# Performance work log

Hardware: AMD Instinct MI355X
Metric: run time of the kernel (lower is better)

## Reference

```python
import jax, jax.numpy as jnp
import numpy as np

NUM_HEADS = 12


def setup_inputs() -> dict:
    key = jax.random.key(0)
    k1, k2, k3, k4 = jax.random.split(key, 4)
    B, N, C = 8, 1024, 768
    x = jax.random.normal(k1, (B, N, C), dtype=jnp.float32)
    w_qkv = jax.random.normal(k2, (3 * C, C), dtype=jnp.float32) * 0.02
    w_proj = jax.random.normal(k3, (C, C), dtype=jnp.float32) * 0.02
    b_proj = jax.random.normal(k4, (C,), dtype=jnp.float32) * 0.02
    return {"x": x, "w_qkv": w_qkv, "w_proj": w_proj, "b_proj": b_proj}


def reference(x, w_qkv, w_proj, b_proj):
    B, N, C = x.shape
    H = NUM_HEADS
    D = C // H
    scale = D ** -0.5
    # qkv projection (HMQLinear with quant=False is a plain linear, bias=False)
    qkv = jnp.einsum('bnc,oc->bno', x, w_qkv)          # [B,N,3C]
    qkv = qkv.reshape(B, N, 3, H, D).transpose(2, 0, 3, 1, 4)  # [3,B,H,N,D]
    q, k, v = qkv[0], qkv[1], qkv[2]
    # HMQMulQK (passthrough matmul), scale applied after QK^T as in source
    attn = jnp.einsum('bhqd,bhkd->bhqk', q, k) * scale  # [B,H,N,N]
    attn = jax.nn.softmax(attn, axis=-1)                # HMQSoftmax
    out = jnp.einsum('bhqk,bhkd->bhqd', attn, v)        # HMQMulSV
    out = out.transpose(0, 2, 1, 3).reshape(B, N, C)
    # output projection (HMQLinear, default bias=True)
    return jnp.einsum('bnc,oc->bno', out, w_proj) + b_proj
```

## Files before the change

kernel.cpp:

```cpp
#include <hip/hip_runtime.h>
#include <hip/hip_bf16.h>
#include <stdint.h>

typedef __attribute__((ext_vector_type(8))) short short8;
typedef __attribute__((ext_vector_type(4))) float f32x4;
typedef __attribute__((ext_vector_type(16))) float f32x16;
typedef __attribute__((ext_vector_type(4))) unsigned short us4;

#define AS1 __attribute__((address_space(1)))
#define AS3 __attribute__((address_space(3)))

__device__ inline unsigned short f2bf(float f) {
    unsigned int u = __float_as_uint(f);
    u += 0x7FFFu + ((u >> 16) & 1u);
    return (unsigned short)(u >> 16);
}

__device__ inline unsigned int cvtpk(float lo, float hi) {
    unsigned int r;
    asm("v_cvt_pk_bf16_f32 %0, %1, %2" : "=v"(r) : "v"(lo), "v"(hi));
    return r;
}

__device__ inline void pl32swap(unsigned int& a, unsigned int& b) {
    asm volatile("v_permlane32_swap_b32 %0, %1" : "+v"(a), "+v"(b));
}

__device__ inline float fexp2(float x) {
#if __has_builtin(__builtin_amdgcn_exp2f)
    return __builtin_amdgcn_exp2f(x);
#else
    return exp2f(x);
#endif
}

#define VMW(N) asm volatile("s_waitcnt vmcnt(" #N ")" ::: "memory")
#define BARR() __builtin_amdgcn_s_barrier()

__global__ void cvt_all(const float* __restrict__ x, const float* __restrict__ wq,
                        const float* __restrict__ wp,
                        unsigned short* __restrict__ xb,
                        unsigned short* __restrict__ wqb,
                        unsigned short* __restrict__ wpb) {
    const int X4 = 1572864, Q4 = 442368;
    int i = blockIdx.x * blockDim.x + threadIdx.x;
    const float* src; unsigned short* dst; int j;
    if (i < X4) { src = x; dst = xb; j = i; }
    else if (i < X4 + Q4) { src = wq; dst = wqb; j = i - X4; }
    else { src = wp; dst = wpb; j = i - X4 - Q4; }
    float4 v = ((const float4*)src)[j];
    us4 o;
    o.x = f2bf(v.x); o.y = f2bf(v.y); o.z = f2bf(v.z); o.w = f2bf(v.w);
    ((us4*)dst)[j] = o;
}

#define BM 128
#define BN 128

template<int MODE>
__global__ __launch_bounds__(256)
void gemm_bt(const unsigned short* __restrict__ A,
             const unsigned short* __restrict__ Bm,
             unsigned short* __restrict__ Qo, unsigned short* __restrict__ Ko,
             unsigned short* __restrict__ Vto,
             float* __restrict__ Co, const float* __restrict__ bias,
             int M, int N, int K)
{
    __shared__ __align__(16) unsigned short As[2][BM * 64];
    __shared__ __align__(16) unsigned short Bs[2][BM * 64];
    const int tid = threadIdx.x;
    const int wave = tid >> 6, lane = tid & 63;
    const int tr = blockIdx.x * BM;
    const int tc = blockIdx.y * BN;
    const int wm = wave >> 1, wn = wave & 1;

    f32x4 acc[4][4] = {};

    auto stage = [&](int it, int buf) {
#pragma unroll
        for (int i = 0; i < 4; ++i) {
            int cid = i * 256 + tid;
            int r = cid >> 3, cd = cid & 7;
            int sc = cd ^ (r & 7);
            __builtin_amdgcn_global_load_lds(
                (const AS1 void*)(A + (size_t)(tr + r) * K + it * 64 + sc * 8),
                (AS3 void*)(&As[buf][(i * 256 + wave * 64) * 8]), 16, 0, 0);
            __builtin_amdgcn_global_load_lds(
                (const AS1 void*)(Bm + (size_t)(tc + r) * K + it * 64 + sc * 8),
                (AS3 void*)(&Bs[buf][(i * 256 + wave * 64) * 8]), 16, 0, 0);
        }
    };

    const int nIt = K / 64;
    stage(0, 0);

    for (int it = 0; it < nIt; ++it) {
        const int cur = it & 1;
        if (it + 1 < nIt) { stage(it + 1, cur ^ 1); VMW(8); }
        else              { VMW(0); }
        BARR();

#pragma unroll
        for (int kh = 0; kh < 2; ++kh) {
            short8 af[4], bfr[4];
#pragma unroll
            for (int mt = 0; mt < 4; ++mt) {
                int rr = wm * 64 + mt * 16 + (lane & 15);
                int c = kh * 4 + (lane >> 4);
                af[mt] = *(const short8*)&As[cur][rr * 64 + ((c ^ (rr & 7)) * 8)];
            }
#pragma unroll
            for (int nt = 0; nt < 4; ++nt) {
                int rr = wn * 64 + nt * 16 + (lane & 15);
                int c = kh * 4 + (lane >> 4);
                bfr[nt] = *(const short8*)&Bs[cur][rr * 64 + ((c ^ (rr & 7)) * 8)];
            }
#pragma unroll
            for (int mt = 0; mt < 4; ++mt)
#pragma unroll
                for (int nt = 0; nt < 4; ++nt)
                    acc[mt][nt] = __builtin_amdgcn_mfma_f32_16x16x32_bf16(af[mt], bfr[nt], acc[mt][nt], 0, 0, 0);
        }

        BARR();
    }

    const float QSCALE = 0.18033688011112042f;
#pragma unroll
    for (int mt = 0; mt < 4; ++mt) {
#pragma unroll
        for (int nt = 0; nt < 4; ++nt) {
            int col = tc + wn * 64 + nt * 16 + (lane & 15);
            int row0 = tr + wm * 64 + mt * 16 + (lane >> 4) * 4;
            if constexpr (MODE == 0) {
                int s = (col >= 1536) ? 2 : (col >= 768 ? 1 : 0);
                int rem = col - s * 768;
                int h = rem >> 6, d = rem & 63;
                int b = row0 >> 10, n0 = row0 & 1023;
                int bh = b * 12 + h;
                if (s == 2) {
                    us4 pv;
#pragma unroll
                    for (int r = 0; r < 4; ++r) pv[r] = f2bf(acc[mt][nt][r]);
                    int qd = (n0 >> 2) & 3;
                    int nst = n0 + ((qd == 1) ? 4 : (qd == 2) ? -4 : 0);
                    *(us4*)&Vto[((size_t)bh * 64 + d) * 1024 + nst] = pv;
                } else {
                    unsigned short* dst = (s == 0) ? Qo : Ko;
                    float sc = (s == 0) ? QSCALE : 1.0f;
#pragma unroll
                    for (int r = 0; r < 4; ++r)
                        dst[((size_t)bh * 1024 + n0 + r) * 64 + d] = f2bf(acc[mt][nt][r] * sc);
                }
            } else {
#pragma unroll
                for (int r = 0; r < 4; ++r)
                    Co[(size_t)(row0 + r) * N + col] = acc[mt][nt][r] + bias[col];
            }
        }
    }
}

__global__ __launch_bounds__(256, 3)
void attn_kernel(const unsigned short* __restrict__ Q,
                 const unsigned short* __restrict__ Kg,
                 const unsigned short* __restrict__ Vt,
                 unsigned short* __restrict__ Og)
{
    __shared__ __align__(16) unsigned short KV[3][2][64 * 64];

    const int tid = threadIdx.x;
    const int wave = tid >> 6, lane = tid & 63;
    const int l31 = lane & 31, hi = lane >> 5;

    const int id = blockIdx.x;
    const int swz = (id & 7) * 96 + (id >> 3);
    const int bh = swz >> 3, qb = swz & 7;

    const int b = bh / 12, h = bh % 12;
    const size_t baseK = (size_t)bh * 1024 * 64;
    const size_t baseV = (size_t)bh * 64 * 1024;
    const int q0 = qb * 128 + wave * 32;

    short8 qf[4];
#pragma unroll
    for (int ds = 0; ds < 4; ++ds)
        qf[ds] = *(const short8*)&Q[baseK + (size_t)(q0 + l31) * 64 + ds * 16 + hi * 8];

    f32x16 ot0 = {}, ot1 = {};
    float l = 0.f;

    auto stage = [&](int kt, int buf) {
        const unsigned short* gK = Kg + baseK + (size_t)kt * 64 * 64;
        const unsigned short* gV = Vt + baseV + kt * 64;
#pragma unroll
        for (int i = 0; i < 2; ++i) {
            int c = wave * 128 + i * 64 + lane;
            int r = c >> 3, cc = c & 7;
            int sw = (cc ^ (r & 7)) * 8;
            __builtin_amdgcn_global_load_lds(
                (const AS1 void*)(gK + r * 64 + sw),
                (AS3 void*)(&KV[buf][0][(wave * 128 + i * 64) * 8]), 16, 0, 0);
            __builtin_amdgcn_global_load_lds(
                (const AS1 void*)(gV + (size_t)r * 1024 + sw),
                (AS3 void*)(&KV[buf][1][(wave * 128 + i * 64) * 8]), 16, 0, 0);
        }
    };

    auto rfrag = [&](const unsigned short* s, int row, int cc) -> short8 {
        return *(const short8*)&s[(row * 8 + (cc ^ (row & 7))) * 8];
    };

    auto pack8 = [&](const f32x16& S, int r0) -> short8 {
        union { unsigned int u[4]; short8 s; } fr;
#pragma unroll
        for (int w = 0; w < 4; ++w)
            fr.u[w] = cvtpk(S[r0 + 2 * w], S[r0 + 2 * w + 1]);
        return fr.s;
    };

    stage(0, 0);
    stage(1, 1);
    int cb = 0, sb = 2;

    for (int kt = 0; kt < 16; ++kt) {
        if (kt < 15) { VMW(4); }
        else         { VMW(0); }
        BARR();
        if (kt < 14) stage(kt + 2, sb);

        f32x16 st0 = {}, st1 = {};
        __builtin_amdgcn_s_setprio(1);
#pragma unroll
        for (int ds = 0; ds < 4; ++ds) {
            short8 k0 = rfrag(KV[cb][0], l31, ds * 2 + hi);
            short8 k1 = rfrag(KV[cb][0], 32 + l31, ds * 2 + hi);
            st0 = __builtin_amdgcn_mfma_f32_32x32x16_bf16(k0, qf[ds], st0, 0, 0, 0);
            st1 = __builtin_amdgcn_mfma_f32_32x32x16_bf16(k1, qf[ds], st1, 0, 0, 0);
        }
        __builtin_amdgcn_s_setprio(0);

        short8 v00 = rfrag(KV[cb][1], l31, 0 + hi);
        short8 v10 = rfrag(KV[cb][1], 32 + l31, 0 + hi);
        short8 v01 = rfrag(KV[cb][1], l31, 2 + hi);
        short8 v11 = rfrag(KV[cb][1], 32 + l31, 2 + hi);

#pragma unroll
        for (int i = 0; i < 16; ++i) st0[i] = fexp2(st0[i]);
        short8 paf0 = pack8(st0, 0);
        short8 paf1 = pack8(st0, 8);

        __builtin_amdgcn_s_setprio(1);
        ot0 = __builtin_amdgcn_mfma_f32_32x32x16_bf16(v00, paf0, ot0, 0, 0, 0);
        ot1 = __builtin_amdgcn_mfma_f32_32x32x16_bf16(v10, paf0, ot1, 0, 0, 0);
        ot0 = __builtin_amdgcn_mfma_f32_32x32x16_bf16(v01, paf1, ot0, 0, 0, 0);
        ot1 = __builtin_amdgcn_mfma_f32_32x32x16_bf16(v11, paf1, ot1, 0, 0, 0);
        __builtin_amdgcn_s_setprio(0);

        short8 v02 = rfrag(KV[cb][1], l31, 4 + hi);
        short8 v12 = rfrag(KV[cb][1], 32 + l31, 4 + hi);
        short8 v03 = rfrag(KV[cb][1], l31, 6 + hi);
        short8 v13 = rfrag(KV[cb][1], 32 + l31, 6 + hi);
#pragma unroll
        for (int i = 0; i < 16; ++i) st1[i] = fexp2(st1[i]);
        short8 paf2 = pack8(st1, 0);
        short8 paf3 = pack8(st1, 8);

        __builtin_amdgcn_s_setprio(1);
        ot0 = __builtin_amdgcn_mfma_f32_32x32x16_bf16(v02, paf2, ot0, 0, 0, 0);
        ot1 = __builtin_amdgcn_mfma_f32_32x32x16_bf16(v12, paf2, ot1, 0, 0, 0);
        ot0 = __builtin_amdgcn_mfma_f32_32x32x16_bf16(v03, paf3, ot0, 0, 0, 0);
        ot1 = __builtin_amdgcn_mfma_f32_32x32x16_bf16(v13, paf3, ot1, 0, 0, 0);
        __builtin_amdgcn_s_setprio(0);

        float su[8];
#pragma unroll
        for (int i = 0; i < 8; ++i)
            su[i] = (st0[2 * i] + st0[2 * i + 1]) + (st1[2 * i] + st1[2 * i + 1]);
#pragma unroll
        for (int s = 4; s > 0; s >>= 1)
#pragma unroll
            for (int i = 0; i < 4; ++i)
                if (i < s) su[i] += su[i + s];
        l += su[0];

        cb = (cb == 2) ? 0 : cb + 1;
        sb = (sb == 2) ? 0 : sb + 1;
    }

    {
        unsigned int pu = __float_as_uint(l), pv = pu;
        pl32swap(pu, pv);
        l += __uint_as_float(hi ? pv : pu);
    }

    float inv = 1.f / l;
#pragma unroll
    for (int i = 0; i < 16; ++i) { ot0[i] *= inv; ot1[i] *= inv; }

    BARR();

    unsigned int* ow = (unsigned int*)(&KV[0][0][0]) + wave * 1152;
#pragma unroll
    for (int dt = 0; dt < 2; ++dt)
#pragma unroll
        for (int rp = 0; rp < 8; ++rp) {
            unsigned int w = (dt == 0) ? cvtpk(ot0[2 * rp], ot0[2 * rp + 1])
                                       : cvtpk(ot1[2 * rp], ot1[2 * rp + 1]);
            int wd = dt * 16 + 4 * (rp >> 1) + 2 * hi + (rp & 1);
            ow[l31 * 36 + wd] = w;
        }
#pragma unroll
    for (int i = 0; i < 4; ++i) {
        int c = i * 64 + lane;
        int qr = c >> 3, ch = c & 7;
        short8 vv = *(const short8*)((const unsigned short*)&ow[qr * 36 + ch * 4]);
        *(short8*)&Og[(size_t)(b * 1024 + q0 + qr) * 768 + h * 64 + ch * 8] = vv;
    }
}

extern "C" void kernel_launch(void* const* d_in, const int* in_sizes, int n_in,
                              void* d_out, int out_size, void* d_ws, size_t ws_size,
                              hipStream_t stream) {
    const float* x      = (const float*)d_in[0];
    const float* w_qkv  = (const float*)d_in[1];
    const float* w_proj = (const float*)d_in[2];
    const float* b_proj = (const float*)d_in[3];
    float* out = (float*)d_out;

    const int Bb = 8, Nn = 1024, C = 768;
    const int M = Bb * Nn;
    const size_t XB = (size_t)M * C;
    const size_t WQ = (size_t)3 * C * C;
    const size_t WP = (size_t)C * C;
    const size_t QE = (size_t)96 * 1024 * 64;

    unsigned short* xb  = (unsigned short*)d_ws;
    unsigned short* wqb = xb + XB;
    unsigned short* wpb = wqb + WQ;
    unsigned short* Qb  = wpb + WP;
    unsigned short* Kb  = Qb + QE;
    unsigned short* Vtb = Kb + QE;
    unsigned short* AO  = Vtb + QE;

    cvt_all<<<8448, 256, 0, stream>>>(x, w_qkv, w_proj, xb, wqb, wpb);

    gemm_bt<0><<<dim3(M / BM, (3 * C) / BN), 256, 0, stream>>>(
        xb, wqb, Qb, Kb, Vtb, nullptr, nullptr, M, 3 * C, C);

    attn_kernel<<<768, 256, 0, stream>>>(Qb, Kb, Vtb, AO);

    gemm_bt<1><<<dim3(M / BM, C / BN), 256, 0, stream>>>(
        AO, wpb, nullptr, nullptr, nullptr, out, b_proj, M, C, C);
}
```

Before: 109.5 us.

## Process two 32-row query tiles per wave in attention, halving block size

The attention block drops from four waves to two, and each wave now handles 64 query rows as two 32-row groups. Each K/V fragment read from LDS is reused across both groups, which halves LDS fragment traffic per unit of MFMA work and gives more independent MFMAs to interleave. The cost is a roughly doubled set of accumulator and score registers per wave (launch bounds change to 128,2), fewer waves per block to hide latency, and each wave issuing twice as many staging loads.

Measured after the change: 112.0 us. 2.3% more time.

```diff
diff --git a/kernel.cpp b/kernel.cpp
--- a/kernel.cpp
+++ b/kernel.cpp
@@ -161,7 +161,7 @@
     }
 }
 
-__global__ __launch_bounds__(256, 3)
+__global__ __launch_bounds__(128, 2)
 void attn_kernel(const unsigned short* __restrict__ Q,
                  const unsigned short* __restrict__ Kg,
                  const unsigned short* __restrict__ Vt,
@@ -180,30 +180,33 @@
     const int b = bh / 12, h = bh % 12;
     const size_t baseK = (size_t)bh * 1024 * 64;
     const size_t baseV = (size_t)bh * 64 * 1024;
-    const int q0 = qb * 128 + wave * 32;
-
-    short8 qf[4];
-#pragma unroll
-    for (int ds = 0; ds < 4; ++ds)
-        qf[ds] = *(const short8*)&Q[baseK + (size_t)(q0 + l31) * 64 + ds * 16 + hi * 8];
-
-    f32x16 ot0 = {}, ot1 = {};
-    float l = 0.f;
+    const int q0A = qb * 128 + wave * 64;
+    const int q0B = q0A + 32;
+
+    short8 qfA[4], qfB[4];
+#pragma unroll
+    for (int ds = 0; ds < 4; ++ds) {
+        qfA[ds] = *(const short8*)&Q[baseK + (size_t)(q0A + l31) * 64 + ds * 16 + hi * 8];
+        qfB[ds] = *(const short8*)&Q[baseK + (size_t)(q0B + l31) * 64 + ds * 16 + hi * 8];
+    }
+
+    f32x16 oA0 = {}, oA1 = {}, oB0 = {}, oB1 = {};
+    float lA = 0.f, lB = 0.f;
 
     auto stage = [&](int kt, int buf) {
         const unsigned short* gK = Kg + baseK + (size_t)kt * 64 * 64;
         const unsigned short* gV = Vt + baseV + kt * 64;
 #pragma unroll
-        for (int i = 0; i < 2; ++i) {
-            int c = wave * 128 + i * 64 + lane;
+        for (int i = 0; i < 4; ++i) {
+            int c = i * 128 + wave * 64 + lane;
             int r = c >> 3, cc = c & 7;
             int sw = (cc ^ (r & 7)) * 8;
             __builtin_amdgcn_global_load_lds(
                 (const AS1 void*)(gK + r * 64 + sw),
-                (AS3 void*)(&KV[buf][0][(wave * 128 + i * 64) * 8]), 16, 0, 0);
+                (AS3 void*)(&KV[buf][0][(i * 128 + wave * 64) * 8]), 16, 0, 0);
             __builtin_amdgcn_global_load_lds(
                 (const AS1 void*)(gV + (size_t)r * 1024 + sw),
-                (AS3 void*)(&KV[buf][1][(wave * 128 + i * 64) * 8]), 16, 0, 0);
+                (AS3 void*)(&KV[buf][1][(i * 128 + wave * 64) * 8]), 16, 0, 0);
         }
     };
 
@@ -224,98 +227,115 @@
     int cb = 0, sb = 2;
 
     for (int kt = 0; kt < 16; ++kt) {
-        if (kt < 15) { VMW(4); }
+        if (kt < 15) { VMW(8); }
         else         { VMW(0); }
         BARR();
         if (kt < 14) stage(kt + 2, sb);
 
-        f32x16 st0 = {}, st1 = {};
+        f32x16 sA0 = {}, sA1 = {}, sB0 = {}, sB1 = {};
         __builtin_amdgcn_s_setprio(1);
 #pragma unroll
         for (int ds = 0; ds < 4; ++ds) {
             short8 k0 = rfrag(KV[cb][0], l31, ds * 2 + hi);
             short8 k1 = rfrag(KV[cb][0], 32 + l31, ds * 2 + hi);
-            st0 = __builtin_amdgcn_mfma_f32_32x32x16_bf16(k0, qf[ds], st0, 0, 0, 0);
-            st1 = __builtin_amdgcn_mfma_f32_32x32x16_bf16(k1, qf[ds], st1, 0, 0, 0);
+            sA0 = __builtin_amdgcn_mfma_f32_32x32x16_bf16(k0, qfA[ds], sA0, 0, 0, 0);
+            sA1 = __builtin_amdgcn_mfma_f32_32x32x16_bf16(k1, qfA[ds], sA1, 0, 0, 0);
+            sB0 = __builtin_amdgcn_mfma_f32_32x32x16_bf16(k0, qfB[ds], sB0, 0, 0, 0);
+            sB1 = __builtin_amdgcn_mfma_f32_32x32x16_bf16(k1, qfB[ds], sB1, 0, 0, 0);
         }
         __builtin_amdgcn_s_setprio(0);
 
-        short8 v00 = rfrag(KV[cb][1], l31, 0 + hi);
-        short8 v10 = rfrag(KV[cb][1], 32 + l31, 0 + hi);
-        short8 v01 = rfrag(KV[cb][1], l31, 2 + hi);
-        short8 v11 = rfrag(KV[cb][1], 32 + l31, 2 + hi);
-
-#pragma unroll
-        for (int i = 0; i < 16; ++i) st0[i] = fexp2(st0[i]);
-        short8 paf0 = pack8(st0, 0);
-        short8 paf1 = pack8(st0, 8);
+        short8 pafA[4], pafB[4];
+#pragma unroll
+        for (int i = 0; i < 16; ++i) { sA0[i] = fexp2(sA0[i]); sA1[i] = fexp2(sA1[i]); }
+        pafA[0] = pack8(sA0, 0); pafA[1] = pack8(sA0, 8);
+        pafA[2] = pack8(sA1, 0); pafA[3] = pack8(sA1, 8);
+        {
+            float su[8];
+#pragma unroll
+            for (int i = 0; i < 8; ++i)
+                su[i] = (sA0[2 * i] + sA0[2 * i + 1]) + (sA1[2 * i] + sA1[2 * i + 1]);
+#pragma unroll
+            for (int s = 4; s > 0; s >>= 1)
+#pragma unroll
+                for (int i = 0; i < 4; ++i)
+                    if (i < s) su[i] += su[i + s];
+            lA += su[0];
+        }
+#pragma unroll
+        for (int i = 0; i < 16; ++i) { sB0[i] = fexp2(sB0[i]); sB1[i] = fexp2(sB1[i]); }
+        pafB[0] = pack8(sB0, 0); pafB[1] = pack8(sB0, 8);
+        pafB[2] = pack8(sB1, 0); pafB[3] = pack8(sB1, 8);
+        {
+            float su[8];
+#pragma unroll
+            for (int i = 0; i < 8; ++i)
+                su[i] = (sB0[2 * i] + sB0[2 * i + 1]) + (sB1[2 * i] + sB1[2 * i + 1]);
+#pragma unroll
+            for (int s = 4; s > 0; s >>= 1)
+#pragma unroll
+                for (int i = 0; i < 4; ++i)
+                    if (i < s) su[i] += su[i + s];
+            lB += su[0];
+        }
 
         __builtin_amdgcn_s_setprio(1);
-        ot0 = __builtin_amdgcn_mfma_f32_32x32x16_bf16(v00, paf0, ot0, 0, 0, 0);
-        ot1 = __builtin_amdgcn_mfma_f32_32x32x16_bf16(v10, paf0, ot1, 0, 0, 0);
-        ot0 = __builtin_amdgcn_mfma_f32_32x32x16_bf16(v01, paf1, ot0, 0, 0, 0);
-        ot1 = __builtin_amdgcn_mfma_f32_32x32x16_bf16(v11, paf1, ot1, 0, 0, 0);
+#pragma unroll
+        for (int kb = 0; kb < 4; ++kb) {
+            short8 v0 = rfrag(KV[cb][1], l31, kb * 2 + hi);
+            short8 v1 = rfrag(KV[cb][1], 32 + l31, kb * 2 + hi);
+            oA0 = __builtin_amdgcn_mfma_f32_32x32x16_bf16(v0, pafA[kb], oA0, 0, 0, 0);
+            oA1 = __builtin_amdgcn_mfma_f32_32x32x16_bf16(v1, pafA[kb], oA1, 0, 0, 0);
+            oB0 = __builtin_amdgcn_mfma_f32_32x32x16_bf16(v0, pafB[kb], oB0, 0, 0, 0);
+            oB1 = __builtin_amdgcn_mfma_f32_32x32x16_bf16(v1, pafB[kb], oB1, 0, 0, 0);
+        }
         __builtin_amdgcn_s_setprio(0);
-
-        short8 v02 = rfrag(KV[cb][1], l31, 4 + hi);
-        short8 v12 = rfrag(KV[cb][1], 32 + l31, 4 + hi);
-        short8 v03 = rfrag(KV[cb][1], l31, 6 + hi);
-        short8 v13 = rfrag(KV[cb][1], 32 + l31, 6 + hi);
-#pragma unroll
-        for (int i = 0; i < 16; ++i) st1[i] = fexp2(st1[i]);
-        short8 paf2 = pack8(st1, 0);
-        short8 paf3 = pack8(st1, 8);
-
-        __builtin_amdgcn_s_setprio(1);
-        ot0 = __builtin_amdgcn_mfma_f32_32x32x16_bf16(v02, paf2, ot0, 0, 0, 0);
-        ot1 = __builtin_amdgcn_mfma_f32_32x32x16_bf16(v12, paf2, ot1, 0, 0, 0);
-        ot0 = __builtin_amdgcn_mfma_f32_32x32x16_bf16(v03, paf3, ot0, 0, 0, 0);
-        ot1 = __builtin_amdgcn_mfma_f32_32x32x16_bf16(v13, paf3, ot1, 0, 0, 0);
-        __builtin_amdgcn_s_setprio(0);
-
-        float su[8];
-#pragma unroll
-        for (int i = 0; i < 8; ++i)
-            su[i] = (st0[2 * i] + st0[2 * i + 1]) + (st1[2 * i] + st1[2 * i + 1]);
-#pragma unroll
-        for (int s = 4; s > 0; s >>= 1)
-#pragma unroll
-            for (int i = 0; i < 4; ++i)
-                if (i < s) su[i] += su[i + s];
-        l += su[0];
 
         cb = (cb == 2) ? 0 : cb + 1;
         sb = (sb == 2) ? 0 : sb + 1;
     }
 
     {
-        unsigned int pu = __float_as_uint(l), pv = pu;
+        unsigned int pu = __float_as_uint(lA), pv = pu;
         pl32swap(pu, pv);
-        l += __uint_as_float(hi ? pv : pu);
-    }
-
-    float inv = 1.f / l;
-#pragma unroll
-    for (int i = 0; i < 16; ++i) { ot0[i] *= inv; ot1[i] *= inv; }
+        lA += __uint_as_float(hi ? pv : pu);
+        unsigned int qu = __float_as_uint(lB), qv = qu;
+        pl32swap(qu, qv);
+        lB += __uint_as_float(hi ? qv : qu);
+    }
+
+    float invA = 1.f / lA, invB = 1.f / lB;
+#pragma unroll
+    for (int i = 0; i < 16; ++i) {
+        oA0[i] *= invA; oA1[i] *= invA;
+        oB0[i] *= invB; oB1[i] *= invB;
+    }
 
     BARR();
 
-    unsigned int* ow = (unsigned int*)(&KV[0][0][0]) + wave * 1152;
-#pragma unroll
-    for (int dt = 0; dt < 2; ++dt)
-#pragma unroll
-        for (int rp = 0; rp < 8; ++rp) {
-            unsigned int w = (dt == 0) ? cvtpk(ot0[2 * rp], ot0[2 * rp + 1])
-                                       : cvtpk(ot1[2 * rp], ot1[2 * rp + 1]);
-            int wd = dt * 16 + 4 * (rp >> 1) + 2 * hi + (rp & 1);
-            ow[l31 * 36 + wd] = w;
-        }
-#pragma unroll
-    for (int i = 0; i < 4; ++i) {
-        int c = i * 64 + lane;
-        int qr = c >> 3, ch = c & 7;
-        short8 vv = *(const short8*)((const unsigned short*)&ow[qr * 36 + ch * 4]);
-        *(short8*)&Og[(size_t)(b * 1024 + q0 + qr) * 768 + h * 64 + ch * 8] = vv;
+    unsigned int* base = (unsigned int*)(&KV[0][0][0]);
+#pragma unroll
+    for (int grp = 0; grp < 2; ++grp) {
+        unsigned int* ow = base + (wave * 2 + grp) * 1152;
+        const f32x16& o0 = grp ? oB0 : oA0;
+        const f32x16& o1 = grp ? oB1 : oA1;
+        const int q0 = grp ? q0B : q0A;
+#pragma unroll
+        for (int dt = 0; dt < 2; ++dt)
+#pragma unroll
+            for (int rp = 0; rp < 8; ++rp) {
+                unsigned int w = (dt == 0) ? cvtpk(o0[2 * rp], o0[2 * rp + 1])
+                                           : cvtpk(o1[2 * rp], o1[2 * rp + 1]);
+                int wd = dt * 16 + 4 * (rp >> 1) + 2 * hi + (rp & 1);
+                ow[l31 * 36 + wd] = w;
+            }
+#pragma unroll
+        for (int i = 0; i < 4; ++i) {
+            int c = i * 64 + lane;
+            int qr = c >> 3, ch = c & 7;
+            short8 vv = *(const short8*)((const unsigned short*)&ow[qr * 36 + ch * 4]);
+            *(short8*)&Og[(size_t)(b * 1024 + q0 + qr) * 768 + h * 64 + ch * 8] = vv;
+        }
     }
 }
 
@@ -348,7 +368,7 @@
     gemm_bt<0><<<dim3(M / BM, (3 * C) / BN), 256, 0, stream>>>(
         xb, wqb, Qb, Kb, Vtb, nullptr, nullptr, M, 3 * C, C);
 
-    attn_kernel<<<768, 256, 0, stream>>>(Qb, Kb, Vtb, AO);
+    attn_kernel<<<768, 128, 0, stream>>>(Qb, Kb, Vtb, AO);
 
     gemm_bt<1><<<dim3(M / BM, C / BN), 256, 0, stream>>>(
         AO, wpb, nullptr, nullptr, nullptr, out, b_proj, M, C, C);
```
